# Optimization experiments

Hardware: AMD Instinct MI355X
Metric: run time of the kernel (lower is better)

## Reference

```python
import jax, jax.numpy as jnp
import numpy as np

VOCAB = 28996
EMBED = 512
N = 8192


def setup_inputs() -> dict:
    key = jax.random.key(0)
    k1, k2, k3, k4 = jax.random.split(key, 4)
    x = jax.random.normal(k1, (N, EMBED), dtype=jnp.float32)
    y = jax.random.randint(k2, (N,), 0, VOCAB, dtype=jnp.int64 if jax.config.jax_enable_x64 else jnp.int32)
    # nn.Linear params: weight (vocab, embed), bias (vocab,)
    W = jax.random.normal(k3, (VOCAB, EMBED), dtype=jnp.float32) * 0.02
    b = jax.random.normal(k4, (VOCAB,), dtype=jnp.float32) * 0.02
    return {"x": x, "y": y, "W": W, "b": b}


def reference(x, y, W, b):
    # Decoder: linear -> softmax over vocab (dim=1)
    logits = jnp.einsum("ne,ve->nv", x, W) + b          # (N, VOCAB)
    probs = jax.nn.softmax(logits, axis=1)              # first softmax (faithful to original)
    # nn.CrossEntropyLoss applied to probs: mean over nodes of
    #   logsumexp(probs) - probs[y]   (i.e., -log_softmax(probs)[y])
    logp = jax.nn.log_softmax(probs, axis=1)            # second (redundant) softmax pass
    nll = -jnp.take_along_axis(logp, y[:, None].astype(jnp.int32), axis=1)[:, 0]
    return jnp.mean(nll)
```

## Files before the change

kernel.cpp:

```cpp
#include <hip/hip_runtime.h>
#include <stdint.h>

#define VOCAB 28996
#define EMBED 512
#define NROWS 8192
#define VPAD  29056
#define LOG2E 1.4426950408889634f
#define WSCALE 16.0f
#define INV_WSCALE_L2E (LOG2E / 16.0f)

typedef __attribute__((ext_vector_type(4)))  int   i32x4;
typedef __attribute__((ext_vector_type(8)))  int   i32x8;
typedef __attribute__((ext_vector_type(16))) float f32x16;

__device__ __forceinline__ void gload_lds16(const void* g, void* l) {
  __builtin_amdgcn_global_load_lds(
      (__attribute__((address_space(1))) const void*)g,
      (__attribute__((address_space(3))) void*)l, 16, 0, 0);
}

__device__ __forceinline__ int pk_fp8x4(float a, float b, float c, float d) {
  int r = __builtin_amdgcn_cvt_pk_fp8_f32(a, b, 0, false);
  r = __builtin_amdgcn_cvt_pk_fp8_f32(c, d, r, true);
  return r;
}

__global__ void __launch_bounds__(256)
prep_kernel(const float* __restrict__ x, const float* __restrict__ W,
            const float* __restrict__ b, const int* __restrict__ y,
            int* __restrict__ xb, int* __restrict__ wb,
            float* __restrict__ py, float* __restrict__ sg) {
  const int bid = blockIdx.x;
  if (bid < 7264) {
    int i = (bid * 256 + threadIdx.x) * 8;
    const int VK = VOCAB * EMBED;
    int2 o;
    if (i < VK) {
      float4 v0 = *(const float4*)(W + i);
      float4 v1 = *(const float4*)(W + i + 4);
      o.x = pk_fp8x4(v0.x * WSCALE, v0.y * WSCALE, v0.z * WSCALE, v0.w * WSCALE);
      o.y = pk_fp8x4(v1.x * WSCALE, v1.y * WSCALE, v1.z * WSCALE, v1.w * WSCALE);
    } else { o.x = 0; o.y = 0; }
    *(int2*)(wb + i / 4) = o;
  } else if (bid < 9312) {
    int i = ((bid - 7264) * 256 + threadIdx.x) * 8;
    float4 v0 = *(const float4*)(x + i);
    float4 v1 = *(const float4*)(x + i + 4);
    int2 o;
    o.x = pk_fp8x4(v0.x, v0.y, v0.z, v0.w);
    o.y = pk_fp8x4(v1.x, v1.y, v1.z, v1.w);
    *(int2*)(xb + i / 4) = o;
  } else if (bid < 11360) {
    const int row  = ((bid - 9312) * 256 + threadIdx.x) >> 6;
    const int lane = threadIdx.x & 63;
    const int yr = y[row];
    const float4* xr = (const float4*)(x + (size_t)row * EMBED);
    const float4* wr = (const float4*)(W + (size_t)yr * EMBED);
    float d = 0.f;
#pragma unroll
    for (int t = 0; t < 2; ++t) {
      float4 a = xr[lane * 2 + t], c = wr[lane * 2 + t];
      d += a.x * c.x + a.y * c.y + a.z * c.z + a.w * c.w;
    }
#pragma unroll
    for (int m = 1; m < 64; m <<= 1) d += __shfl_xor(d, m);
    if (lane == 0) py[row] = __expf(d + b[yr]);
  } else {
    int i = (bid - 11360) * 256 + threadIdx.x;
    sg[i] = 0.f;
  }
}

__global__ void __launch_bounds__(256, 4)
gemm_stats_kernel(const uint8_t* __restrict__ xb, const uint8_t* __restrict__ wb,
                  const float* __restrict__ bias, float* __restrict__ sg) {
  __shared__ uint8_t lA[128 * 128];
  __shared__ uint8_t lB[128 * 128];

  const int tid  = threadIdx.x;
  const int lane = tid & 63;
  const int w    = tid >> 6;
  const int l31  = lane & 31;
  const int h    = lane >> 5;
  const int kx   = lane & 7;
  const int wr   = (w >> 1) * 64;
  const int wc   = (w & 1) * 64;
  const int rowBase = blockIdx.x * 128;
  const int colBase = blockIdx.y * 128;

  f32x16 acc[2][2];
#pragma unroll
  for (int i = 0; i < 2; ++i)
#pragma unroll
    for (int j = 0; j < 2; ++j)
#pragma unroll
      for (int r = 0; r < 16; ++r) acc[i][j][r] = 0.f;

  const int srow = lane >> 3;
  const int skel = ((lane & 7) ^ srow) * 16;

  const int aBase = (wr + l31) * 128;
  const int bBase = (wc + l31) * 128;

  for (int kt = 0; kt < 4; ++kt) {
    const int k0 = kt * 128;
#pragma unroll
    for (int t = 0; t < 4; ++t) {
      const int c = w * 4 + t;
      const int r = c * 8 + srow;
      gload_lds16(xb + (size_t)(rowBase + r) * EMBED + k0 + skel, &lA[c * 1024]);
      gload_lds16(wb + (size_t)(colBase + r) * EMBED + k0 + skel, &lB[c * 1024]);
    }
    __syncthreads();
#pragma unroll
    for (int kk = 0; kk < 2; ++kk) {
      const int c0 = ((kk * 4 + h * 2) ^ kx) << 4;
      const int c1 = c0 ^ 16;
      i32x8 bq[2];
#pragma unroll
      for (int jj = 0; jj < 2; ++jj) {
        const int base = bBase + jj * 32 * 128;
        i32x4 lo = *(const i32x4*)&lB[base + c0];
        i32x4 hi = *(const i32x4*)&lB[base + c1];
        bq[jj] = __builtin_shufflevector(lo, hi, 0, 1, 2, 3, 4, 5, 6, 7);
      }
#pragma unroll
      for (int ii = 0; ii < 2; ++ii) {
        const int base = aBase + ii * 32 * 128;
        i32x4 lo = *(const i32x4*)&lA[base + c0];
        i32x4 hi = *(const i32x4*)&lA[base + c1];
        i32x8 af = __builtin_shufflevector(lo, hi, 0, 1, 2, 3, 4, 5, 6, 7);
        acc[ii][0] = __builtin_amdgcn_mfma_scale_f32_32x32x64_f8f6f4(
            af, bq[0], acc[ii][0], 0, 0, 0, 0x7F7F7F7F, 0, 0x7F7F7F7F);
        acc[ii][1] = __builtin_amdgcn_mfma_scale_f32_32x32x64_f8f6f4(
            af, bq[1], acc[ii][1], 0, 0, 0, 0x7F7F7F7F, 0, 0x7F7F7F7F);
      }
    }
    __syncthreads();
  }

  float bvl[2];
#pragma unroll
  for (int jj = 0; jj < 2; ++jj) {
    const int col = colBase + wc + jj * 32 + l31;
    bvl[jj] = (col < VOCAB) ? bias[col] * LOG2E : -1e30f;
  }

  float sp[32];
#pragma unroll
  for (int ii = 0; ii < 2; ++ii)
#pragma unroll
    for (int r = 0; r < 16; ++r)
      sp[ii * 16 + r] = exp2f(fmaf(acc[ii][0][r], INV_WSCALE_L2E, bvl[0])) +
                        exp2f(fmaf(acc[ii][1][r], INV_WSCALE_L2E, bvl[1]));

  float t1[16];
#pragma unroll
  for (int u = 0; u < 16; ++u) {
    float a = sp[2 * u]     + __shfl_xor(sp[2 * u],     1);
    float b = sp[2 * u + 1] + __shfl_xor(sp[2 * u + 1], 1);
    t1[u] = (l31 & 1) ? b : a;
  }
  float t2[8];
#pragma unroll
  for (int u = 0; u < 8; ++u) {
    float a = t1[2 * u]     + __shfl_xor(t1[2 * u],     2);
    float b = t1[2 * u + 1] + __shfl_xor(t1[2 * u + 1], 2);
    t2[u] = (l31 & 2) ? b : a;
  }
  float t3[4];
#pragma unroll
  for (int u = 0; u < 4; ++u) {
    float a = t2[2 * u]     + __shfl_xor(t2[2 * u],     4);
    float b = t2[2 * u + 1] + __shfl_xor(t2[2 * u + 1], 4);
    t3[u] = (l31 & 4) ? b : a;
  }
  float t4[2];
#pragma unroll
  for (int u = 0; u < 2; ++u) {
    float a = t3[2 * u]     + __shfl_xor(t3[2 * u],     8);
    float b = t3[2 * u + 1] + __shfl_xor(t3[2 * u + 1], 8);
    t4[u] = (l31 & 8) ? b : a;
  }
  {
    float a = t4[0] + __shfl_xor(t4[0], 16);
    float b = t4[1] + __shfl_xor(t4[1], 16);
    float ssum = (l31 & 16) ? b : a;
    const int v = l31;
    const int row = rowBase + wr + (v >> 4) * 32 + (v & 3) + 8 * ((v & 15) >> 2) + 4 * h;
    atomicAdd(&sg[row], ssum);
  }
}

__global__ void finalize_kernel(const float* __restrict__ sg, const float* __restrict__ py,
                                float* __restrict__ out) {
  __shared__ float red[256];
  float a = 0.f;
  for (int i = threadIdx.x; i < NROWS; i += 256)
    a += py[i] / sg[i];
  red[threadIdx.x] = a;
  __syncthreads();
  for (int st = 128; st > 0; st >>= 1) {
    if (threadIdx.x < st) red[threadIdx.x] += red[threadIdx.x + st];
    __syncthreads();
  }
  if (threadIdx.x == 0)
    out[0] = logf((float)(VOCAB + 1)) - red[0] * (1.f / (float)NROWS);
}

extern "C" void kernel_launch(void* const* d_in, const int* in_sizes, int n_in,
                              void* d_out, int out_size, void* d_ws, size_t ws_size,
                              hipStream_t stream) {
  const float* x = (const float*)d_in[0];
  const int*   y = (const int*)d_in[1];
  const float* W = (const float*)d_in[2];
  const float* b = (const float*)d_in[3];

  char* ws = (char*)d_ws;
  uint8_t* xb = (uint8_t*)ws;
  uint8_t* wb = (uint8_t*)(ws + 4194304);
  float*   sg = (float*)(ws + 4194304 + 14876672);
  float*   py = sg + NROWS;

  prep_kernel<<<11392, 256, 0, stream>>>(x, W, b, y, (int*)xb, (int*)wb, py, sg);
  gemm_stats_kernel<<<dim3(64, 227), 256, 0, stream>>>(xb, wb, b, sg);
  finalize_kernel<<<1, 256, 0, stream>>>(sg, py, (float*)d_out);
}
```

Before: 281.9 us.

## Enlarge GEMM tile to 256x256 with double-buffered LDS and MFMA priority

Moves the fp8 GEMM+softmax-stats kernel from 128x128 tiles with 4 waves to 256x256 tiles with 8 waves, each wave holding a 128x64 accumulator block. The aim is to halve global and LDS traffic per FLOP by reusing each loaded tile across more output. Shared memory is double-buffered, so the next K slice's global-to-LDS loads are issued while the current slice is multiplied, and one barrier per K step is removed. MFMA issue is wrapped in s_setprio. In exchange it uses about 128KB of LDS and more accumulator registers, which allows only one block per CU. It also clamps weight-row loads for the padded last column tile, which adds some wasted work there.

```diff
diff --git a/kernel.cpp b/kernel.cpp
--- a/kernel.cpp
+++ b/kernel.cpp
@@ -71,11 +71,11 @@
   }
 }
 
-__global__ void __launch_bounds__(256, 4)
+__global__ void __launch_bounds__(512, 2)
 gemm_stats_kernel(const uint8_t* __restrict__ xb, const uint8_t* __restrict__ wb,
                   const float* __restrict__ bias, float* __restrict__ sg) {
-  __shared__ uint8_t lA[128 * 128];
-  __shared__ uint8_t lB[128 * 128];
+  __shared__ uint8_t lA[2][256 * 128];
+  __shared__ uint8_t lB[2][256 * 128];
 
   const int tid  = threadIdx.x;
   const int lane = tid & 63;
@@ -83,112 +83,135 @@
   const int l31  = lane & 31;
   const int h    = lane >> 5;
   const int kx   = lane & 7;
-  const int wr   = (w >> 1) * 64;
-  const int wc   = (w & 1) * 64;
-  const int rowBase = blockIdx.x * 128;
-  const int colBase = blockIdx.y * 128;
-
-  f32x16 acc[2][2];
-#pragma unroll
-  for (int i = 0; i < 2; ++i)
+  const int wr   = (w >> 2) * 128;
+  const int wc   = (w & 3) * 64;
+  const int rowBase = blockIdx.x * 256;
+  const int colBase = blockIdx.y * 256;
+
+  const int srow = lane >> 3;
+  const int skel = (kx ^ srow) * 16;
+
+  f32x16 acc[4][2];
+#pragma unroll
+  for (int i = 0; i < 4; ++i)
 #pragma unroll
     for (int j = 0; j < 2; ++j)
 #pragma unroll
       for (int r = 0; r < 16; ++r) acc[i][j][r] = 0.f;
 
-  const int srow = lane >> 3;
-  const int skel = ((lane & 7) ^ srow) * 16;
+  auto stage = [&](int buf, int k0) {
+#pragma unroll
+    for (int t = 0; t < 4; ++t) {
+      const int c = w * 4 + t;
+      const int ar = rowBase + c * 8;
+      int br = colBase + c * 8;
+      if (br > VPAD - 8) br = VPAD - 8;
+      gload_lds16(xb + (size_t)(ar + srow) * EMBED + k0 + skel, &lA[buf][c * 1024]);
+      gload_lds16(wb + (size_t)(br + srow) * EMBED + k0 + skel, &lB[buf][c * 1024]);
+    }
+  };
+
+  stage(0, 0);
 
   const int aBase = (wr + l31) * 128;
   const int bBase = (wc + l31) * 128;
 
+#pragma unroll
   for (int kt = 0; kt < 4; ++kt) {
-    const int k0 = kt * 128;
-#pragma unroll
-    for (int t = 0; t < 4; ++t) {
-      const int c = w * 4 + t;
-      const int r = c * 8 + srow;
-      gload_lds16(xb + (size_t)(rowBase + r) * EMBED + k0 + skel, &lA[c * 1024]);
-      gload_lds16(wb + (size_t)(colBase + r) * EMBED + k0 + skel, &lB[c * 1024]);
-    }
+    const int cur = kt & 1;
     __syncthreads();
+    if (kt < 3) stage(cur ^ 1, (kt + 1) * 128);
+    i32x8 bq[2][2];
 #pragma unroll
     for (int kk = 0; kk < 2; ++kk) {
       const int c0 = ((kk * 4 + h * 2) ^ kx) << 4;
       const int c1 = c0 ^ 16;
-      i32x8 bq[2];
-#pragma unroll
-      for (int jj = 0; jj < 2; ++jj) {
-        const int base = bBase + jj * 32 * 128;
-        i32x4 lo = *(const i32x4*)&lB[base + c0];
-        i32x4 hi = *(const i32x4*)&lB[base + c1];
-        bq[jj] = __builtin_shufflevector(lo, hi, 0, 1, 2, 3, 4, 5, 6, 7);
+#pragma unroll
+      for (int ni = 0; ni < 2; ++ni) {
+        const uint8_t* bp = &lB[cur][bBase + ni * 32 * 128];
+        i32x4 lo = *(const i32x4*)(bp + c0);
+        i32x4 hi = *(const i32x4*)(bp + c1);
+        bq[kk][ni] = __builtin_shufflevector(lo, hi, 0, 1, 2, 3, 4, 5, 6, 7);
       }
-#pragma unroll
-      for (int ii = 0; ii < 2; ++ii) {
-        const int base = aBase + ii * 32 * 128;
-        i32x4 lo = *(const i32x4*)&lA[base + c0];
-        i32x4 hi = *(const i32x4*)&lA[base + c1];
-        i32x8 af = __builtin_shufflevector(lo, hi, 0, 1, 2, 3, 4, 5, 6, 7);
-        acc[ii][0] = __builtin_amdgcn_mfma_scale_f32_32x32x64_f8f6f4(
-            af, bq[0], acc[ii][0], 0, 0, 0, 0x7F7F7F7F, 0, 0x7F7F7F7F);
-        acc[ii][1] = __builtin_amdgcn_mfma_scale_f32_32x32x64_f8f6f4(
-            af, bq[1], acc[ii][1], 0, 0, 0, 0x7F7F7F7F, 0, 0x7F7F7F7F);
+    }
+#pragma unroll
+    for (int mi = 0; mi < 4; ++mi) {
+      i32x8 af[2];
+#pragma unroll
+      for (int kk = 0; kk < 2; ++kk) {
+        const int c0 = ((kk * 4 + h * 2) ^ kx) << 4;
+        const int c1 = c0 ^ 16;
+        const uint8_t* ap = &lA[cur][aBase + mi * 32 * 128];
+        i32x4 lo = *(const i32x4*)(ap + c0);
+        i32x4 hi = *(const i32x4*)(ap + c1);
+        af[kk] = __builtin_shufflevector(lo, hi, 0, 1, 2, 3, 4, 5, 6, 7);
       }
-    }
-    __syncthreads();
+      __builtin_amdgcn_s_setprio(1);
+#pragma unroll
+      for (int kk = 0; kk < 2; ++kk)
+#pragma unroll
+        for (int ni = 0; ni < 2; ++ni)
+          acc[mi][ni] = __builtin_amdgcn_mfma_scale_f32_32x32x64_f8f6f4(
+              af[kk], bq[kk][ni], acc[mi][ni], 0, 0, 0, 0x7F7F7F7F, 0, 0x7F7F7F7F);
+      __builtin_amdgcn_s_setprio(0);
+    }
   }
 
   float bvl[2];
 #pragma unroll
-  for (int jj = 0; jj < 2; ++jj) {
-    const int col = colBase + wc + jj * 32 + l31;
-    bvl[jj] = (col < VOCAB) ? bias[col] * LOG2E : -1e30f;
-  }
-
-  float sp[32];
-#pragma unroll
-  for (int ii = 0; ii < 2; ++ii)
-#pragma unroll
-    for (int r = 0; r < 16; ++r)
-      sp[ii * 16 + r] = exp2f(fmaf(acc[ii][0][r], INV_WSCALE_L2E, bvl[0])) +
-                        exp2f(fmaf(acc[ii][1][r], INV_WSCALE_L2E, bvl[1]));
-
-  float t1[16];
-#pragma unroll
-  for (int u = 0; u < 16; ++u) {
-    float a = sp[2 * u]     + __shfl_xor(sp[2 * u],     1);
-    float b = sp[2 * u + 1] + __shfl_xor(sp[2 * u + 1], 1);
-    t1[u] = (l31 & 1) ? b : a;
-  }
-  float t2[8];
-#pragma unroll
-  for (int u = 0; u < 8; ++u) {
-    float a = t1[2 * u]     + __shfl_xor(t1[2 * u],     2);
-    float b = t1[2 * u + 1] + __shfl_xor(t1[2 * u + 1], 2);
-    t2[u] = (l31 & 2) ? b : a;
-  }
-  float t3[4];
-#pragma unroll
-  for (int u = 0; u < 4; ++u) {
-    float a = t2[2 * u]     + __shfl_xor(t2[2 * u],     4);
-    float b = t2[2 * u + 1] + __shfl_xor(t2[2 * u + 1], 4);
-    t3[u] = (l31 & 4) ? b : a;
-  }
-  float t4[2];
-#pragma unroll
-  for (int u = 0; u < 2; ++u) {
-    float a = t3[2 * u]     + __shfl_xor(t3[2 * u],     8);
-    float b = t3[2 * u + 1] + __shfl_xor(t3[2 * u + 1], 8);
-    t4[u] = (l31 & 8) ? b : a;
-  }
-  {
-    float a = t4[0] + __shfl_xor(t4[0], 16);
-    float b = t4[1] + __shfl_xor(t4[1], 16);
-    float ssum = (l31 & 16) ? b : a;
-    const int v = l31;
-    const int row = rowBase + wr + (v >> 4) * 32 + (v & 3) + 8 * ((v & 15) >> 2) + 4 * h;
-    atomicAdd(&sg[row], ssum);
+  for (int ni = 0; ni < 2; ++ni) {
+    const int col = colBase + wc + ni * 32 + l31;
+    bvl[ni] = (col < VOCAB) ? bias[col] * LOG2E : -1e30f;
+  }
+
+#pragma unroll
+  for (int p = 0; p < 2; ++p) {
+    float sp[32];
+#pragma unroll
+    for (int q = 0; q < 2; ++q)
+#pragma unroll
+      for (int r = 0; r < 16; ++r)
+        sp[q * 16 + r] =
+            exp2f(fmaf(acc[p * 2 + q][0][r], INV_WSCALE_L2E, bvl[0])) +
+            exp2f(fmaf(acc[p * 2 + q][1][r], INV_WSCALE_L2E, bvl[1]));
+
+    float t1[16];
+#pragma unroll
+    for (int u = 0; u < 16; ++u) {
+      float a = sp[2 * u]     + __shfl_xor(sp[2 * u],     1);
+      float b = sp[2 * u + 1] + __shfl_xor(sp[2 * u + 1], 1);
+      t1[u] = (l31 & 1) ? b : a;
+    }
+    float t2[8];
+#pragma unroll
+    for (int u = 0; u < 8; ++u) {
+      float a = t1[2 * u]     + __shfl_xor(t1[2 * u],     2);
+      float b = t1[2 * u + 1] + __shfl_xor(t1[2 * u + 1], 2);
+      t2[u] = (l31 & 2) ? b : a;
+    }
+    float t3[4];
+#pragma unroll
+    for (int u = 0; u < 4; ++u) {
+      float a = t2[2 * u]     + __shfl_xor(t2[2 * u],     4);
+      float b = t2[2 * u + 1] + __shfl_xor(t2[2 * u + 1], 4);
+      t3[u] = (l31 & 4) ? b : a;
+    }
+    float t4[2];
+#pragma unroll
+    for (int u = 0; u < 2; ++u) {
+      float a = t3[2 * u]     + __shfl_xor(t3[2 * u],     8);
+      float b = t3[2 * u + 1] + __shfl_xor(t3[2 * u + 1], 8);
+      t4[u] = (l31 & 8) ? b : a;
+    }
+    {
+      float a = t4[0] + __shfl_xor(t4[0], 16);
+      float b = t4[1] + __shfl_xor(t4[1], 16);
+      float ssum = (l31 & 16) ? b : a;
+      const int v = l31;
+      const int row = rowBase + wr + p * 64 + (v >> 4) * 32 +
+                      (v & 3) + 8 * ((v & 15) >> 2) + 4 * h;
+      atomicAdd(&sg[row], ssum);
+    }
   }
 }
 
@@ -223,6 +246,6 @@
   float*   py = sg + NROWS;
 
   prep_kernel<<<11392, 256, 0, stream>>>(x, W, b, y, (int*)xb, (int*)wb, py, sg);
-  gemm_stats_kernel<<<dim3(64, 227), 256, 0, stream>>>(xb, wb, b, sg);
+  gemm_stats_kernel<<<dim3(32, 114), 512, 0, stream>>>(xb, wb, b, sg);
   finalize_kernel<<<1, 256, 0, stream>>>(sg, py, (float*)d_out);
 }
```

Measured after the change: 314.2 us. 11.4% more time.

## Double-buffer LDS tiles with K=64 stages to overlap loads with MFMA

Applied to the files above, without the earlier changes.

Splits the K loop into eight 64-wide stages and ping-pongs two LDS buffers, so the next stage's global-to-LDS load is issued before the current stage's MFMAs run. This targets the exposed load latency of the old single-buffer loop, which synced, computed and synced again. The swizzle is reworked for 64-byte rows. Total LDS stays the same, but each stage is smaller, which adds per-stage barriers. One barrier per stage may not guard against async global_load_lds writes still in flight.

```diff
diff --git a/kernel.cpp b/kernel.cpp
--- a/kernel.cpp
+++ b/kernel.cpp
@@ -74,20 +74,22 @@
 __global__ void __launch_bounds__(256, 4)
 gemm_stats_kernel(const uint8_t* __restrict__ xb, const uint8_t* __restrict__ wb,
                   const float* __restrict__ bias, float* __restrict__ sg) {
-  __shared__ uint8_t lA[128 * 128];
-  __shared__ uint8_t lB[128 * 128];
+  __shared__ uint8_t lA[2][128 * 64];
+  __shared__ uint8_t lB[2][128 * 64];
 
   const int tid  = threadIdx.x;
   const int lane = tid & 63;
   const int w    = tid >> 6;
   const int l31  = lane & 31;
   const int h    = lane >> 5;
-  const int kx   = lane & 7;
   const int wr   = (w >> 1) * 64;
   const int wc   = (w & 1) * 64;
   const int rowBase = blockIdx.x * 128;
   const int colBase = blockIdx.y * 128;
 
+  const int ric  = lane >> 2;
+  const int slt  = ((lane & 3) ^ (ric & 3)) * 16;
+
   f32x16 acc[2][2];
 #pragma unroll
   for (int i = 0; i < 2; ++i)
@@ -96,47 +98,49 @@
 #pragma unroll
       for (int r = 0; r < 16; ++r) acc[i][j][r] = 0.f;
 
-  const int srow = lane >> 3;
-  const int skel = ((lane & 7) ^ srow) * 16;
-
-  const int aBase = (wr + l31) * 128;
-  const int bBase = (wc + l31) * 128;
-
-  for (int kt = 0; kt < 4; ++kt) {
-    const int k0 = kt * 128;
-#pragma unroll
-    for (int t = 0; t < 4; ++t) {
-      const int c = w * 4 + t;
-      const int r = c * 8 + srow;
-      gload_lds16(xb + (size_t)(rowBase + r) * EMBED + k0 + skel, &lA[c * 1024]);
-      gload_lds16(wb + (size_t)(colBase + r) * EMBED + k0 + skel, &lB[c * 1024]);
-    }
+  auto stage = [&](int buf, int k0) {
+#pragma unroll
+    for (int t = 0; t < 2; ++t) {
+      const int c = w * 2 + t;
+      gload_lds16(xb + (size_t)(rowBase + c * 16 + ric) * EMBED + k0 + slt,
+                  &lA[buf][c * 1024]);
+      gload_lds16(wb + (size_t)(colBase + c * 16 + ric) * EMBED + k0 + slt,
+                  &lB[buf][c * 1024]);
+    }
+  };
+
+  stage(0, 0);
+
+  const int aBase = (wr + l31) * 64;
+  const int bBase = (wc + l31) * 64;
+  const int c0    = ((h * 2) ^ (l31 & 3)) << 4;
+  const int c1    = c0 ^ 16;
+
+#pragma unroll
+  for (int kt = 0; kt < 8; ++kt) {
+    const int cur = kt & 1;
     __syncthreads();
-#pragma unroll
-    for (int kk = 0; kk < 2; ++kk) {
-      const int c0 = ((kk * 4 + h * 2) ^ kx) << 4;
-      const int c1 = c0 ^ 16;
-      i32x8 bq[2];
-#pragma unroll
-      for (int jj = 0; jj < 2; ++jj) {
-        const int base = bBase + jj * 32 * 128;
-        i32x4 lo = *(const i32x4*)&lB[base + c0];
-        i32x4 hi = *(const i32x4*)&lB[base + c1];
-        bq[jj] = __builtin_shufflevector(lo, hi, 0, 1, 2, 3, 4, 5, 6, 7);
-      }
-#pragma unroll
-      for (int ii = 0; ii < 2; ++ii) {
-        const int base = aBase + ii * 32 * 128;
-        i32x4 lo = *(const i32x4*)&lA[base + c0];
-        i32x4 hi = *(const i32x4*)&lA[base + c1];
-        i32x8 af = __builtin_shufflevector(lo, hi, 0, 1, 2, 3, 4, 5, 6, 7);
-        acc[ii][0] = __builtin_amdgcn_mfma_scale_f32_32x32x64_f8f6f4(
-            af, bq[0], acc[ii][0], 0, 0, 0, 0x7F7F7F7F, 0, 0x7F7F7F7F);
-        acc[ii][1] = __builtin_amdgcn_mfma_scale_f32_32x32x64_f8f6f4(
-            af, bq[1], acc[ii][1], 0, 0, 0, 0x7F7F7F7F, 0, 0x7F7F7F7F);
-      }
-    }
-    __syncthreads();
+    if (kt < 7) stage(cur ^ 1, (kt + 1) * 64);
+
+    i32x8 bq[2];
+#pragma unroll
+    for (int jj = 0; jj < 2; ++jj) {
+      const uint8_t* bp = &lB[cur][bBase + jj * 32 * 64];
+      i32x4 lo = *(const i32x4*)(bp + c0);
+      i32x4 hi = *(const i32x4*)(bp + c1);
+      bq[jj] = __builtin_shufflevector(lo, hi, 0, 1, 2, 3, 4, 5, 6, 7);
+    }
+#pragma unroll
+    for (int ii = 0; ii < 2; ++ii) {
+      const uint8_t* ap = &lA[cur][aBase + ii * 32 * 64];
+      i32x4 lo = *(const i32x4*)(ap + c0);
+      i32x4 hi = *(const i32x4*)(ap + c1);
+      i32x8 af = __builtin_shufflevector(lo, hi, 0, 1, 2, 3, 4, 5, 6, 7);
+      acc[ii][0] = __builtin_amdgcn_mfma_scale_f32_32x32x64_f8f6f4(
+          af, bq[0], acc[ii][0], 0, 0, 0, 0x7F7F7F7F, 0, 0x7F7F7F7F);
+      acc[ii][1] = __builtin_amdgcn_mfma_scale_f32_32x32x64_f8f6f4(
+          af, bq[1], acc[ii][1], 0, 0, 0, 0x7F7F7F7F, 0, 0x7F7F7F7F);
+    }
   }
 
   float bvl[2];
```

Result: slower. 296.9 us (+5.3%).

## Load GEMM fragments directly from global memory into registers, bypassing LDS

Applied to the files above, without the earlier changes.

The FP8 GEMM no longer stages the A and B tiles through shared memory with global_load_lds and barriers. Each lane now loads its MFMA operand fragments straight from global into registers, with the K loop fully unrolled, and the occupancy hint drops from 4 to 3 blocks. The goal is to remove LDS traffic and __syncthreads stalls, at the cost of redundant global and L2 reads, since neighbouring waves re-fetch the same rows, plus higher register pressure. The finalize reduction also grows from 256 to 1024 threads.

```diff
diff --git a/kernel.cpp b/kernel.cpp
--- a/kernel.cpp
+++ b/kernel.cpp
@@ -9,15 +9,8 @@
 #define WSCALE 16.0f
 #define INV_WSCALE_L2E (LOG2E / 16.0f)
 
-typedef __attribute__((ext_vector_type(4)))  int   i32x4;
 typedef __attribute__((ext_vector_type(8)))  int   i32x8;
 typedef __attribute__((ext_vector_type(16))) float f32x16;
-
-__device__ __forceinline__ void gload_lds16(const void* g, void* l) {
-  __builtin_amdgcn_global_load_lds(
-      (__attribute__((address_space(1))) const void*)g,
-      (__attribute__((address_space(3))) void*)l, 16, 0, 0);
-}
 
 __device__ __forceinline__ int pk_fp8x4(float a, float b, float c, float d) {
   int r = __builtin_amdgcn_cvt_pk_fp8_f32(a, b, 0, false);
@@ -71,23 +64,22 @@
   }
 }
 
-__global__ void __launch_bounds__(256, 4)
+__global__ void __launch_bounds__(256, 3)
 gemm_stats_kernel(const uint8_t* __restrict__ xb, const uint8_t* __restrict__ wb,
                   const float* __restrict__ bias, float* __restrict__ sg) {
-  __shared__ uint8_t lA[128 * 128];
-  __shared__ uint8_t lB[128 * 128];
-
   const int tid  = threadIdx.x;
   const int lane = tid & 63;
   const int w    = tid >> 6;
   const int l31  = lane & 31;
   const int h    = lane >> 5;
-  const int kx   = lane & 7;
   const int wr   = (w >> 1) * 64;
   const int wc   = (w & 1) * 64;
   const int rowBase = blockIdx.x * 128;
   const int colBase = blockIdx.y * 128;
 
+  const uint8_t* pa = xb + (size_t)(rowBase + wr + l31) * EMBED + h * 32;
+  const uint8_t* pb = wb + (size_t)(colBase + wc + l31) * EMBED + h * 32;
+
   f32x16 acc[2][2];
 #pragma unroll
   for (int i = 0; i < 2; ++i)
@@ -96,47 +88,29 @@
 #pragma unroll
       for (int r = 0; r < 16; ++r) acc[i][j][r] = 0.f;
 
-  const int srow = lane >> 3;
-  const int skel = ((lane & 7) ^ srow) * 16;
-
-  const int aBase = (wr + l31) * 128;
-  const int bBase = (wc + l31) * 128;
-
+#pragma unroll
   for (int kt = 0; kt < 4; ++kt) {
-    const int k0 = kt * 128;
-#pragma unroll
-    for (int t = 0; t < 4; ++t) {
-      const int c = w * 4 + t;
-      const int r = c * 8 + srow;
-      gload_lds16(xb + (size_t)(rowBase + r) * EMBED + k0 + skel, &lA[c * 1024]);
-      gload_lds16(wb + (size_t)(colBase + r) * EMBED + k0 + skel, &lB[c * 1024]);
-    }
-    __syncthreads();
-#pragma unroll
-    for (int kk = 0; kk < 2; ++kk) {
-      const int c0 = ((kk * 4 + h * 2) ^ kx) << 4;
-      const int c1 = c0 ^ 16;
-      i32x8 bq[2];
-#pragma unroll
-      for (int jj = 0; jj < 2; ++jj) {
-        const int base = bBase + jj * 32 * 128;
-        i32x4 lo = *(const i32x4*)&lB[base + c0];
-        i32x4 hi = *(const i32x4*)&lB[base + c1];
-        bq[jj] = __builtin_shufflevector(lo, hi, 0, 1, 2, 3, 4, 5, 6, 7);
+    const int ko = kt * 128;
+    i32x8 bq[2][2], aq[2][2];
+#pragma unroll
+    for (int kk = 0; kk < 2; ++kk)
+#pragma unroll
+      for (int jj = 0; jj < 2; ++jj)
+        bq[kk][jj] = *(const i32x8*)(pb + jj * (32 * EMBED) + ko + kk * 64);
+#pragma unroll
+    for (int kk = 0; kk < 2; ++kk)
+#pragma unroll
+      for (int ii = 0; ii < 2; ++ii)
+        aq[kk][ii] = *(const i32x8*)(pa + ii * (32 * EMBED) + ko + kk * 64);
+#pragma unroll
+    for (int kk = 0; kk < 2; ++kk)
+#pragma unroll
+      for (int ii = 0; ii < 2; ++ii) {
+        acc[ii][0] = __builtin_amdgcn_mfma_scale_f32_32x32x64_f8f6f4(
+            aq[kk][ii], bq[kk][0], acc[ii][0], 0, 0, 0, 0x7F7F7F7F, 0, 0x7F7F7F7F);
+        acc[ii][1] = __builtin_amdgcn_mfma_scale_f32_32x32x64_f8f6f4(
+            aq[kk][ii], bq[kk][1], acc[ii][1], 0, 0, 0, 0x7F7F7F7F, 0, 0x7F7F7F7F);
       }
-#pragma unroll
-      for (int ii = 0; ii < 2; ++ii) {
-        const int base = aBase + ii * 32 * 128;
-        i32x4 lo = *(const i32x4*)&lA[base + c0];
-        i32x4 hi = *(const i32x4*)&lA[base + c1];
-        i32x8 af = __builtin_shufflevector(lo, hi, 0, 1, 2, 3, 4, 5, 6, 7);
-        acc[ii][0] = __builtin_amdgcn_mfma_scale_f32_32x32x64_f8f6f4(
-            af, bq[0], acc[ii][0], 0, 0, 0, 0x7F7F7F7F, 0, 0x7F7F7F7F);
-        acc[ii][1] = __builtin_amdgcn_mfma_scale_f32_32x32x64_f8f6f4(
-            af, bq[1], acc[ii][1], 0, 0, 0, 0x7F7F7F7F, 0, 0x7F7F7F7F);
-      }
-    }
-    __syncthreads();
   }
 
   float bvl[2];
@@ -192,15 +166,16 @@
   }
 }
 
-__global__ void finalize_kernel(const float* __restrict__ sg, const float* __restrict__ py,
-                                float* __restrict__ out) {
-  __shared__ float red[256];
+__global__ void __launch_bounds__(1024)
+finalize_kernel(const float* __restrict__ sg, const float* __restrict__ py,
+                float* __restrict__ out) {
+  __shared__ float red[1024];
   float a = 0.f;
-  for (int i = threadIdx.x; i < NROWS; i += 256)
+  for (int i = threadIdx.x; i < NROWS; i += 1024)
     a += py[i] / sg[i];
   red[threadIdx.x] = a;
   __syncthreads();
-  for (int st = 128; st > 0; st >>= 1) {
+  for (int st = 512; st > 0; st >>= 1) {
     if (threadIdx.x < st) red[threadIdx.x] += red[threadIdx.x + st];
     __syncthreads();
   }
@@ -224,5 +199,5 @@
 
   prep_kernel<<<11392, 256, 0, stream>>>(x, W, b, y, (int*)xb, (int*)wb, py, sg);
   gemm_stats_kernel<<<dim3(64, 227), 256, 0, stream>>>(xb, wb, b, sg);
-  finalize_kernel<<<1, 256, 0, stream>>>(sg, py, (float*)d_out);
-}
+  finalize_kernel<<<1, 1024, 0, stream>>>(sg, py, (float*)d_out);
+}
```

Result: slower. 518.6 us (+83.9%).
